# Kernel tuning notes

Hardware: AMD Instinct MI355X
Metric: run time of the kernel (lower is better)

## Reference

```python
import jax, jax.numpy as jnp
import numpy as np

B, S, D = 16, 1024, 512
H = 2048
E = 16
TOP_K = 4


def setup_inputs() -> dict:
    key = jax.random.key(0)
    ks = jax.random.split(key, 8)
    scale = 0.02
    x = jax.random.normal(ks[0], (B, S, D), dtype=jnp.float32)
    router_w = jax.random.normal(ks[1], (D, E), dtype=jnp.float32) * scale
    router_b = jax.random.normal(ks[2], (E,), dtype=jnp.float32) * scale
    w1 = jax.random.normal(ks[3], (E, D, H), dtype=jnp.float32) * scale
    b1 = jax.random.normal(ks[4], (E, H), dtype=jnp.float32) * scale
    w2 = jax.random.normal(ks[5], (E, H, D), dtype=jnp.float32) * scale
    b2 = jax.random.normal(ks[6], (E, D), dtype=jnp.float32) * scale
    return {"x": x, "router_w": router_w, "router_b": router_b,
            "w1": w1, "b1": b1, "w2": w2, "b2": b2}


def reference(x, router_w, router_b, w1, b1, w2, b2):
    # x: [B, S, D] -> flatten tokens
    x_flat = x.reshape(-1, D)                       # [T, D]
    logits = x_flat @ router_w + router_b           # [T, E]
    top_vals, top_idx = jax.lax.top_k(logits, TOP_K)  # [T, K]
    gates = jax.nn.softmax(top_vals, axis=-1)       # softmax over selected experts only
    # Combined per-expert gate weight per token: sum over k slots routed to e.
    onehot = jax.nn.one_hot(top_idx, E, dtype=x.dtype)  # [T, K, E]
    comb = jnp.einsum('tk,tke->te', gates, onehot)      # [T, E]
    out = jnp.zeros_like(x_flat)
    for e in range(E):  # fixed small expert count
        h = jax.nn.relu(x_flat @ w1[e] + b1[e])     # [T, H]
        y = h @ w2[e] + b2[e]                       # [T, D]
        out = out + comb[:, e:e + 1] * y
    return out.reshape(x.shape)
```

## Files before the change

### kernel.cpp

```cpp
#include <hip/hip_runtime.h>
#include <stdint.h>

#define T_TOK 16384
#define DIM 512
#define HID 2048
#define NE 16
#define TOPK 4
#define BM 128
#define BN 128
#define BK 64
#define PAIR_CAP 67584
#define MAX_TILES 528
#define NB_CNT 64

typedef short s8v __attribute__((ext_vector_type(8)));
typedef float f4v __attribute__((ext_vector_type(4)));
typedef unsigned int u4v __attribute__((ext_vector_type(4)));

__device__ __forceinline__ unsigned short f2bf(float f) {
  unsigned int u = __builtin_bit_cast(unsigned int, f);
  u = (u + 0x7fffu + ((u >> 16) & 1u)) >> 16;
  return (unsigned short)u;
}
__device__ __forceinline__ float bf2f(unsigned short h) {
  return __builtin_bit_cast(float, (unsigned int)h << 16);
}

__device__ __forceinline__ void gload16(const void* g, void* l) {
  __builtin_amdgcn_global_load_lds(
      (const __attribute__((address_space(1))) unsigned int*)(uintptr_t)g,
      (__attribute__((address_space(3))) unsigned int*)(uintptr_t)l,
      16, 0, 0);
}

__global__ __launch_bounds__(256) void k_transpose_cast(const float* __restrict__ src,
                                                        unsigned short* __restrict__ dst,
                                                        int R, int C) {
  __shared__ float tile[32][33];
  size_t zo = (size_t)blockIdx.z * R * C;
  src += zo; dst += zo;
  int c0 = blockIdx.x * 32, r0 = blockIdx.y * 32;
  int tx = threadIdx.x, ty = threadIdx.y;
#pragma unroll
  for (int i = 0; i < 4; ++i)
    tile[ty + 8 * i][tx] = src[(size_t)(r0 + ty + 8 * i) * C + c0 + tx];
  __syncthreads();
#pragma unroll
  for (int i = 0; i < 4; ++i)
    dst[(size_t)(c0 + ty + 8 * i) * R + r0 + tx] = f2bf(tile[tx][ty + 8 * i]);
}

__global__ __launch_bounds__(256) void k_router(const float* __restrict__ x,
                                                const float* __restrict__ rw,
                                                const float* __restrict__ rb,
                                                int* __restrict__ topki,
                                                float* __restrict__ topkg,
                                                unsigned short* __restrict__ xb) {
  int wv = threadIdx.x >> 6, lane = threadIdx.x & 63;
  int t = blockIdx.x * 4 + wv;
  const float* xr = x + (size_t)t * DIM;
  unsigned short* xbr = xb + (size_t)t * DIM;
  double acc[NE];
#pragma unroll
  for (int e = 0; e < NE; ++e) acc[e] = 0.0;
  for (int it = 0; it < DIM / 64; ++it) {
    float xv = xr[it * 64 + lane];
    xbr[it * 64 + lane] = f2bf(xv);
    const float* r = rw + (size_t)(it * 64 + lane) * NE;
#pragma unroll
    for (int e = 0; e < NE; ++e) acc[e] += (double)xv * (double)r[e];
  }
#pragma unroll
  for (int off = 32; off >= 1; off >>= 1) {
#pragma unroll
    for (int e = 0; e < NE; ++e) acc[e] += __shfl_xor(acc[e], off, 64);
  }
  if (lane == 0) {
    float v[NE];
#pragma unroll
    for (int e = 0; e < NE; ++e) v[e] = (float)acc[e] + rb[e];
    int idx[TOPK]; float val[TOPK];
#pragma unroll
    for (int k = 0; k < TOPK; ++k) {
      float best = -1e30f; int bi = 0;
#pragma unroll
      for (int e = 0; e < NE; ++e)
        if (v[e] > best) { best = v[e]; bi = e; }
      idx[k] = bi; val[k] = best; v[bi] = -1e30f;
    }
    float m = val[0], s = 0.f, g[TOPK];
#pragma unroll
    for (int k = 0; k < TOPK; ++k) { g[k] = __expf(val[k] - m); s += g[k]; }
    float inv = 1.f / s;
#pragma unroll
    for (int k = 0; k < TOPK; ++k) {
      topki[t * TOPK + k] = idx[k];
      topkg[t * TOPK + k] = g[k] * inv;
    }
  }
}

__global__ __launch_bounds__(256) void k_count(const int* __restrict__ topki,
                                               int* __restrict__ meta) {
  __shared__ int lcnt[NE];
  int tid = threadIdx.x;
  if (tid < NE) lcnt[tid] = 0;
  __syncthreads();
  int base = blockIdx.x * 1024 + tid * 4;
#pragma unroll
  for (int j = 0; j < 4; ++j) atomicAdd(&lcnt[topki[base + j]], 1);
  __syncthreads();
  if (tid < NE) meta[1056 + blockIdx.x * NE + tid] = lcnt[tid];
}

__global__ __launch_bounds__(256) void k_plan(int* __restrict__ meta,
                                              int* __restrict__ ptok,
                                              float* __restrict__ pgate) {
  __shared__ int cnt_s[NE], po_s[NE + 1];
  int tid = threadIdx.x;
  if (tid < NE) {
    int s = 0;
    for (int b = 0; b < NB_CNT; ++b) s += meta[1056 + b * NE + tid];
    cnt_s[tid] = s;
  }
  __syncthreads();
  if (tid == 0) {
    int off = 0;
    for (int e = 0; e < NE; ++e) {
      po_s[e] = off;
      meta[1 + e] = off;
      off += ((cnt_s[e] + BM - 1) / BM) * BM;
    }
    po_s[NE] = off;
    meta[1 + NE] = off;
    meta[0] = off / BM;
  }
  __syncthreads();
  if (tid < NE) {
    int run = po_s[tid];
    for (int b = 0; b < NB_CNT; ++b) {
      meta[32 + b * NE + tid] = run;
      run += meta[1056 + b * NE + tid];
    }
  }
  for (int e = 0; e < NE; ++e) {
    int start = po_s[e] + cnt_s[e], end = po_s[e + 1];
    for (int i = start + tid; i < end; i += 256) { ptok[i] = 0; pgate[i] = 0.f; }
  }
}

__global__ __launch_bounds__(256) void k_scatter(const int* __restrict__ topki,
                                                 const float* __restrict__ topkg,
                                                 const int* __restrict__ meta,
                                                 int* __restrict__ ptok,
                                                 float* __restrict__ pgate,
                                                 int* __restrict__ sinv) {
  __shared__ int lcnt[NE];
  int tid = threadIdx.x;
  if (tid < NE) lcnt[tid] = 0;
  __syncthreads();
  int base = blockIdx.x * 1024 + tid * 4;
#pragma unroll
  for (int j = 0; j < 4; ++j) {
    int i = base + j;
    int e = topki[i];
    int r = atomicAdd(&lcnt[e], 1);
    int slot = meta[32 + blockIdx.x * NE + e] + r;
    ptok[slot] = i >> 2;
    pgate[slot] = topkg[i];
    sinv[i] = slot;
  }
}

__global__ __launch_bounds__(256) void k_pipe(const unsigned short* __restrict__ xb,
                                              const unsigned short* __restrict__ w1t,
                                              const float* __restrict__ b1,
                                              const unsigned short* __restrict__ w2t,
                                              const float* __restrict__ b2,
                                              const int* __restrict__ ptok,
                                              const float* __restrict__ pgate,
                                              const int* __restrict__ meta,
                                              unsigned short* __restrict__ hdst,
                                              const unsigned short* __restrict__ hsrc,
                                              unsigned short* __restrict__ yslot,
                                              float* __restrict__ out,
                                              int c1, int c2, int C) {
  __shared__ __align__(16) unsigned short Al[BM * BK];
  __shared__ __align__(16) unsigned short Bl[BN * BK];
  int tid = threadIdx.x;
  int lane = tid & 63, w = tid >> 6;
  int wm = w >> 1, wn = w & 1;
  int w4 = w * 4096;
  int sub = lane >> 3;
  int lg = (lane & 7) ^ sub;
  int lrow = lane & 15, quad = lane >> 4;
  int r7 = lrow & 7;

  if (blockIdx.x < 16) {
    if (c1 < 0) return;
    int tile = c1 * C + blockIdx.y;
    if (tile >= meta[0]) return;
    int row0 = tile * BM;
    int e = 0;
#pragma unroll
    for (int i = 1; i < NE; ++i)
      if (row0 >= meta[1 + i]) e = i;
    int nblock = blockIdx.x * BN;
    const unsigned short* asrc[4];
    const unsigned short* bsrc[4];
#pragma unroll
    for (int t = 0; t < 4; ++t) {
      int r = w * 32 + t * 8 + sub;
      asrc[t] = xb + (size_t)ptok[row0 + r] * DIM + lg * 8;
      bsrc[t] = w1t + ((size_t)e * HID + nblock + r) * DIM + lg * 8;
    }
    f4v acc[4][4] = {};
    for (int k0 = 0; k0 < DIM; k0 += BK) {
#pragma unroll
      for (int t = 0; t < 4; ++t) gload16(asrc[t] + k0, (char*)Al + w4 + t * 1024);
#pragma unroll
      for (int t = 0; t < 4; ++t) gload16(bsrc[t] + k0, (char*)Bl + w4 + t * 1024);
      __syncthreads();
#pragma unroll
      for (int ks = 0; ks < 2; ++ks) {
        int pg = ((ks * 4 + quad) ^ r7) * 8;
        s8v af[4], bfr[4];
#pragma unroll
        for (int mt = 0; mt < 4; ++mt)
          af[mt] = __builtin_bit_cast(s8v, *(const u4v*)&Al[(wm * 64 + mt * 16 + lrow) * BK + pg]);
#pragma unroll
        for (int nt = 0; nt < 4; ++nt)
          bfr[nt] = __builtin_bit_cast(s8v, *(const u4v*)&Bl[(wn * 64 + nt * 16 + lrow) * BK + pg]);
#pragma unroll
        for (int mt = 0; mt < 4; ++mt) {
#pragma unroll
          for (int nt = 0; nt < 4; ++nt)
            acc[mt][nt] = __builtin_amdgcn_mfma_f32_16x16x32_bf16(af[mt], bfr[nt], acc[mt][nt], 0, 0, 0);
        }
      }
      __syncthreads();
    }
    size_t hrow0 = (size_t)blockIdx.y * BM;
#pragma unroll
    for (int nt = 0; nt < 4; ++nt) {
      int gcol = nblock + wn * 64 + nt * 16 + lrow;
      float bias = b1[e * HID + gcol];
#pragma unroll
      for (int mt = 0; mt < 4; ++mt) {
#pragma unroll
        for (int j = 0; j < 4; ++j) {
          int grow = wm * 64 + mt * 16 + quad * 4 + j;
          float v = acc[mt][nt][j] + bias;
          hdst[(hrow0 + grow) * HID + gcol] = f2bf(v > 0.f ? v : 0.f);
        }
      }
    }
  } else {
    if (c2 < 0) return;
    int tile = c2 * C + blockIdx.y;
    if (tile >= meta[0]) return;
    int row0 = tile * BM;
    int e = 0;
#pragma unroll
    for (int i = 1; i < NE; ++i)
      if (row0 >= meta[1 + i]) e = i;
    int nblock = (blockIdx.x - 16) * BN;
    const unsigned short* asrc[4];
    const unsigned short* bsrc[4];
#pragma unroll
    for (int t = 0; t < 4; ++t) {
      int r = w * 32 + t * 8 + sub;
      asrc[t] = hsrc + ((size_t)blockIdx.y * BM + r) * HID + lg * 8;
      bsrc[t] = w2t + ((size_t)e * DIM + nblock + r) * HID + lg * 8;
    }
    f4v acc[4][4] = {};
    for (int k0 = 0; k0 < HID; k0 += BK) {
#pragma unroll
      for (int t = 0; t < 4; ++t) gload16(asrc[t] + k0, (char*)Al + w4 + t * 1024);
#pragma unroll
      for (int t = 0; t < 4; ++t) gload16(bsrc[t] + k0, (char*)Bl + w4 + t * 1024);
      __syncthreads();
#pragma unroll
      for (int ks = 0; ks < 2; ++ks) {
        int pg = ((ks * 4 + quad) ^ r7) * 8;
        s8v af[4], bfr[4];
#pragma unroll
        for (int mt = 0; mt < 4; ++mt)
          af[mt] = __builtin_bit_cast(s8v, *(const u4v*)&Al[(wm * 64 + mt * 16 + lrow) * BK + pg]);
#pragma unroll
        for (int nt = 0; nt < 4; ++nt)
          bfr[nt] = __builtin_bit_cast(s8v, *(const u4v*)&Bl[(wn * 64 + nt * 16 + lrow) * BK + pg]);
#pragma unroll
        for (int mt = 0; mt < 4; ++mt) {
#pragma unroll
          for (int nt = 0; nt < 4; ++nt)
            acc[mt][nt] = __builtin_amdgcn_mfma_f32_16x16x32_bf16(af[mt], bfr[nt], acc[mt][nt], 0, 0, 0);
        }
      }
      __syncthreads();
    }
    float bias[4];
#pragma unroll
    for (int nt = 0; nt < 4; ++nt)
      bias[nt] = b2[e * DIM + nblock + wn * 64 + nt * 16 + lrow];
    if (yslot) {
#pragma unroll
      for (int mt = 0; mt < 4; ++mt) {
#pragma unroll
        for (int j = 0; j < 4; ++j) {
          int p = row0 + wm * 64 + mt * 16 + quad * 4 + j;
          float g = pgate[p];
          unsigned short* yr = yslot + (size_t)p * DIM + nblock + wn * 64 + lrow;
#pragma unroll
          for (int nt = 0; nt < 4; ++nt)
            yr[nt * 16] = f2bf(g * (acc[mt][nt][j] + bias[nt]));
        }
      }
    } else {
#pragma unroll
      for (int mt = 0; mt < 4; ++mt) {
#pragma unroll
        for (int j = 0; j < 4; ++j) {
          int p = row0 + wm * 64 + mt * 16 + quad * 4 + j;
          float g = pgate[p];
          if (g != 0.f) {
            int tok = ptok[p];
            float* orow = out + (size_t)tok * DIM + nblock + wn * 64 + lrow;
#pragma unroll
            for (int nt = 0; nt < 4; ++nt)
              atomicAdd(orow + nt * 16, g * (acc[mt][nt][j] + bias[nt]));
          }
        }
      }
    }
  }
}

__global__ __launch_bounds__(256) void k_gather(const unsigned short* __restrict__ yslot,
                                                const int* __restrict__ sinv,
                                                float* __restrict__ out) {
  int id = blockIdx.x * 256 + threadIdx.x;
  int t = id >> 7, d4 = (id & 127) << 2;
  int4 s = *(const int4*)(sinv + t * 4);
  int sl[4] = {s.x, s.y, s.z, s.w};
  float sum0 = 0.f, sum1 = 0.f, sum2 = 0.f, sum3 = 0.f;
#pragma unroll
  for (int k = 0; k < 4; ++k) {
    ushort4 v = *(const ushort4*)(yslot + (size_t)sl[k] * DIM + d4);
    sum0 += bf2f(v.x); sum1 += bf2f(v.y); sum2 += bf2f(v.z); sum3 += bf2f(v.w);
  }
  float4 r; r.x = sum0; r.y = sum1; r.z = sum2; r.w = sum3;
  *(float4*)(out + (size_t)t * DIM + d4) = r;
}

extern "C" void kernel_launch(void* const* d_in, const int* in_sizes, int n_in,
                              void* d_out, int out_size, void* d_ws, size_t ws_size,
                              hipStream_t stream) {
  const float* x  = (const float*)d_in[0];
  const float* rw = (const float*)d_in[1];
  const float* rb = (const float*)d_in[2];
  const float* w1 = (const float*)d_in[3];
  const float* b1 = (const float*)d_in[4];
  const float* w2 = (const float*)d_in[5];
  const float* b2 = (const float*)d_in[6];
  float* out = (float*)d_out;
  char* ws = (char*)d_ws;

  size_t o_xb    = 0;
  size_t o_w1t   = o_xb    + (size_t)T_TOK * DIM * 2;
  size_t o_w2t   = o_w1t   + (size_t)NE * DIM * HID * 2;
  size_t o_topki = o_w2t   + (size_t)NE * DIM * HID * 2;
  size_t o_topkg = o_topki + (size_t)T_TOK * TOPK * 4;
  size_t o_meta  = o_topkg + (size_t)T_TOK * TOPK * 4;
  size_t o_ptok  = o_meta  + 16384;
  size_t o_pgate = o_ptok  + (size_t)PAIR_CAP * 4;
  size_t o_sinv  = o_pgate + (size_t)PAIR_CAP * 4;
  size_t o_yslot = o_sinv  + (size_t)T_TOK * TOPK * 4;
  size_t o_hb    = o_yslot + (size_t)PAIR_CAP * DIM * 2;

  unsigned short* xb   = (unsigned short*)(ws + o_xb);
  unsigned short* w1t  = (unsigned short*)(ws + o_w1t);
  unsigned short* w2t  = (unsigned short*)(ws + o_w2t);
  int*            tki  = (int*)(ws + o_topki);
  float*          tkg  = (float*)(ws + o_topkg);
  int*            meta = (int*)(ws + o_meta);
  int*            ptok = (int*)(ws + o_ptok);
  float*          pgt  = (float*)(ws + o_pgate);
  int*            sinv = (int*)(ws + o_sinv);

  size_t tile_h = (size_t)BM * HID * 2;
  size_t avail = ws_size > o_hb ? ws_size - o_hb : 0;
  long Cd = (long)(avail / (2 * tile_h));
  int use_slot = Cd >= 1;

  k_router<<<T_TOK / 4, 256, 0, stream>>>(x, rw, rb, tki, tkg, xb);
  k_transpose_cast<<<dim3(HID / 32, DIM / 32, NE), dim3(32, 8), 0, stream>>>(w1, w1t, DIM, HID);
  k_transpose_cast<<<dim3(DIM / 32, HID / 32, NE), dim3(32, 8), 0, stream>>>(w2, w2t, HID, DIM);
  k_count<<<NB_CNT, 256, 0, stream>>>(tki, meta);
  k_plan<<<1, 256, 0, stream>>>(meta, ptok, pgt);
  k_scatter<<<NB_CNT, 256, 0, stream>>>(tki, tkg, meta, ptok, pgt, sinv);

  if (use_slot) {
    unsigned short* ysl = (unsigned short*)(ws + o_yslot);
    int C = (int)(Cd > MAX_TILES ? MAX_TILES : Cd);
    int n_chunks = (MAX_TILES + C - 1) / C;
    unsigned short* hb0 = (unsigned short*)(ws + o_hb);
    unsigned short* hb1 = hb0 + (size_t)C * BM * HID;
    for (int i = 0; i <= n_chunks; ++i) {
      unsigned short* dst = (i & 1) ? hb1 : hb0;
      unsigned short* src = (i & 1) ? hb0 : hb1;
      int c1 = (i < n_chunks) ? i : -1;
      int c2 = i - 1;
      k_pipe<<<dim3(20, C), 256, 0, stream>>>(xb, w1t, b1, w2t, b2, ptok, pgt, meta,
                                              dst, src, ysl, out, c1, c2, C);
    }
    k_gather<<<T_TOK * DIM / 4 / 256, 256, 0, stream>>>(ysl, sinv, out);
  } else {
    long Cf = (long)((ws_size - o_yslot) / tile_h);
    int C = (int)(Cf < 1 ? 1 : (Cf > MAX_TILES ? MAX_TILES : Cf));
    int n_chunks = (MAX_TILES + C - 1) / C;
    unsigned short* hb = (unsigned short*)(ws + o_yslot);
    hipMemsetAsync(d_out, 0, (size_t)T_TOK * DIM * 4, stream);
    for (int i = 0; i < n_chunks; ++i) {
      k_pipe<<<dim3(20, C), 256, 0, stream>>>(xb, w1t, b1, w2t, b2, ptok, pgt, meta,
                                              hb, hb, nullptr, out, i, -1, C);
      k_pipe<<<dim3(20, C), 256, 0, stream>>>(xb, w1t, b1, w2t, b2, ptok, pgt, meta,
                                              hb, hb, nullptr, out, -1, i, C);
    }
  }
}
```

Baseline: 725.6 us.

## Replace chunked FFN launches with a persistent work-queue kernel and ring buffer

The per-chunk k_pipe launches are replaced by one persistent k_moe kernel of 1024 blocks. Each block takes work items from an atomic counter, and the GEMM2 items for a tile trail the GEMM1 items by LAG tiles. GEMM1 writes ReLU activations into a ring of R tile buffers, and per-tile done counters with acquire/release spin-waits enforce the producer/consumer ordering. This removes the launch boundaries and tail idle time between chunks, so the two GEMM phases can overlap. In exchange it adds spin-wait synchronisation, drops the atomicAdd fallback used when workspace is small, and fails if R becomes zero.

```diff
diff --git a/kernel.cpp b/kernel.cpp
--- a/kernel.cpp
+++ b/kernel.cpp
@@ -13,6 +13,10 @@
 #define MAX_TILES 528
 #define NB_CNT 64
 
+#define MQ_CTR 2080
+#define MQ_G1  2112
+#define MQ_G2  2656
+
 typedef short s8v __attribute__((ext_vector_type(8)));
 typedef float f4v __attribute__((ext_vector_type(4)));
 typedef unsigned int u4v __attribute__((ext_vector_type(4)));
@@ -118,6 +122,7 @@
                                               float* __restrict__ pgate) {
   __shared__ int cnt_s[NE], po_s[NE + 1];
   int tid = threadIdx.x;
+  for (int i = tid; i < 1120; i += 256) meta[MQ_CTR + i] = 0;
   if (tid < NE) {
     int s = 0;
     for (int b = 0; b < NB_CNT; ++b) s += meta[1056 + b * NE + tid];
@@ -172,21 +177,20 @@
   }
 }
 
-__global__ __launch_bounds__(256) void k_pipe(const unsigned short* __restrict__ xb,
-                                              const unsigned short* __restrict__ w1t,
-                                              const float* __restrict__ b1,
-                                              const unsigned short* __restrict__ w2t,
-                                              const float* __restrict__ b2,
-                                              const int* __restrict__ ptok,
-                                              const float* __restrict__ pgate,
-                                              const int* __restrict__ meta,
-                                              unsigned short* __restrict__ hdst,
-                                              const unsigned short* __restrict__ hsrc,
-                                              unsigned short* __restrict__ yslot,
-                                              float* __restrict__ out,
-                                              int c1, int c2, int C) {
+__global__ __launch_bounds__(256, 4) void k_moe(const unsigned short* __restrict__ xb,
+                                                const unsigned short* __restrict__ w1t,
+                                                const float* __restrict__ b1,
+                                                const unsigned short* __restrict__ w2t,
+                                                const float* __restrict__ b2,
+                                                const int* __restrict__ ptok,
+                                                const float* __restrict__ pgate,
+                                                int* meta,
+                                                unsigned short* hring,
+                                                unsigned short* __restrict__ yslot,
+                                                int R, int LAG) {
   __shared__ __align__(16) unsigned short Al[BM * BK];
   __shared__ __align__(16) unsigned short Bl[BN * BK];
+  __shared__ int s_item;
   int tid = threadIdx.x;
   int lane = tid & 63, w = tid >> 6;
   int wm = w >> 1, wn = w & 1;
@@ -195,141 +199,154 @@
   int lg = (lane & 7) ^ sub;
   int lrow = lane & 15, quad = lane >> 4;
   int r7 = lrow & 7;
-
-  if (blockIdx.x < 16) {
-    if (c1 < 0) return;
-    int tile = c1 * C + blockIdx.y;
-    if (tile >= meta[0]) return;
-    int row0 = tile * BM;
-    int e = 0;
-#pragma unroll
-    for (int i = 1; i < NE; ++i)
-      if (row0 >= meta[1 + i]) e = i;
-    int nblock = blockIdx.x * BN;
-    const unsigned short* asrc[4];
-    const unsigned short* bsrc[4];
-#pragma unroll
-    for (int t = 0; t < 4; ++t) {
-      int r = w * 32 + t * 8 + sub;
-      asrc[t] = xb + (size_t)ptok[row0 + r] * DIM + lg * 8;
-      bsrc[t] = w1t + ((size_t)e * HID + nblock + r) * DIM + lg * 8;
-    }
-    f4v acc[4][4] = {};
-    for (int k0 = 0; k0 < DIM; k0 += BK) {
-#pragma unroll
-      for (int t = 0; t < 4; ++t) gload16(asrc[t] + k0, (char*)Al + w4 + t * 1024);
-#pragma unroll
-      for (int t = 0; t < 4; ++t) gload16(bsrc[t] + k0, (char*)Bl + w4 + t * 1024);
+  int tiles = meta[0];
+  int seqlen = (tiles + LAG) * 20;
+  int* g1done = meta + MQ_G1;
+  int* g2done = meta + MQ_G2;
+
+  for (;;) {
+    __syncthreads();
+    if (tid == 0) s_item = atomicAdd(&meta[MQ_CTR], 1);
+    __syncthreads();
+    int p = s_item;
+    if (p >= seqlen) return;
+    int tt = p / 20, r = p % 20;
+    if (r < 16) {
+      if (tt >= tiles) continue;
+      int tile = tt;
+      int row0 = tile * BM;
+      int e = 0;
+#pragma unroll
+      for (int i = 1; i < NE; ++i)
+        if (row0 >= meta[1 + i]) e = i;
+      int nblock = r * BN;
+      const unsigned short* asrc[4];
+      const unsigned short* bsrc[4];
+#pragma unroll
+      for (int t = 0; t < 4; ++t) {
+        int rr = w * 32 + t * 8 + sub;
+        asrc[t] = xb + (size_t)ptok[row0 + rr] * DIM + lg * 8;
+        bsrc[t] = w1t + ((size_t)e * HID + nblock + rr) * DIM + lg * 8;
+      }
+      f4v acc[4][4] = {};
+      for (int k0 = 0; k0 < DIM; k0 += BK) {
+#pragma unroll
+        for (int t = 0; t < 4; ++t) gload16(asrc[t] + k0, (char*)Al + w4 + t * 1024);
+#pragma unroll
+        for (int t = 0; t < 4; ++t) gload16(bsrc[t] + k0, (char*)Bl + w4 + t * 1024);
+        __syncthreads();
+#pragma unroll
+        for (int ks = 0; ks < 2; ++ks) {
+          int pg = ((ks * 4 + quad) ^ r7) * 8;
+          s8v af[4], bfr[4];
+#pragma unroll
+          for (int mt = 0; mt < 4; ++mt)
+            af[mt] = __builtin_bit_cast(s8v, *(const u4v*)&Al[(wm * 64 + mt * 16 + lrow) * BK + pg]);
+#pragma unroll
+          for (int nt = 0; nt < 4; ++nt)
+            bfr[nt] = __builtin_bit_cast(s8v, *(const u4v*)&Bl[(wn * 64 + nt * 16 + lrow) * BK + pg]);
+#pragma unroll
+          for (int mt = 0; mt < 4; ++mt) {
+#pragma unroll
+            for (int nt = 0; nt < 4; ++nt)
+              acc[mt][nt] = __builtin_amdgcn_mfma_f32_16x16x32_bf16(af[mt], bfr[nt], acc[mt][nt], 0, 0, 0);
+          }
+        }
+        __syncthreads();
+      }
+      int prev = tile - R;
+      if (prev >= 0) {
+        if (tid == 0) {
+          while (__hip_atomic_load(&g2done[prev], __ATOMIC_ACQUIRE, __HIP_MEMORY_SCOPE_AGENT) < 4)
+            __builtin_amdgcn_s_sleep(2);
+        }
+        __syncthreads();
+      }
+      unsigned short* hdst = hring + (size_t)(tile % R) * BM * HID;
+#pragma unroll
+      for (int nt = 0; nt < 4; ++nt) {
+        int gcol = nblock + wn * 64 + nt * 16 + lrow;
+        float bias = b1[e * HID + gcol];
+#pragma unroll
+        for (int mt = 0; mt < 4; ++mt) {
+#pragma unroll
+          for (int j = 0; j < 4; ++j) {
+            int grow = wm * 64 + mt * 16 + quad * 4 + j;
+            float v = acc[mt][nt][j] + bias;
+            hdst[(size_t)grow * HID + gcol] = f2bf(v > 0.f ? v : 0.f);
+          }
+        }
+      }
       __syncthreads();
-#pragma unroll
-      for (int ks = 0; ks < 2; ++ks) {
-        int pg = ((ks * 4 + quad) ^ r7) * 8;
-        s8v af[4], bfr[4];
-#pragma unroll
-        for (int mt = 0; mt < 4; ++mt)
-          af[mt] = __builtin_bit_cast(s8v, *(const u4v*)&Al[(wm * 64 + mt * 16 + lrow) * BK + pg]);
-#pragma unroll
-        for (int nt = 0; nt < 4; ++nt)
-          bfr[nt] = __builtin_bit_cast(s8v, *(const u4v*)&Bl[(wn * 64 + nt * 16 + lrow) * BK + pg]);
-#pragma unroll
-        for (int mt = 0; mt < 4; ++mt) {
+      if (tid == 0) {
+        __threadfence();
+        __hip_atomic_fetch_add(&g1done[tile], 1, __ATOMIC_RELEASE, __HIP_MEMORY_SCOPE_AGENT);
+      }
+    } else {
+      int tile = tt - LAG;
+      if (tile < 0 || tile >= tiles) continue;
+      int row0 = tile * BM;
+      int e = 0;
+#pragma unroll
+      for (int i = 1; i < NE; ++i)
+        if (row0 >= meta[1 + i]) e = i;
+      int nblock = (r - 16) * BN;
+      if (tid == 0) {
+        while (__hip_atomic_load(&g1done[tile], __ATOMIC_ACQUIRE, __HIP_MEMORY_SCOPE_AGENT) < 16)
+          __builtin_amdgcn_s_sleep(2);
+      }
+      __syncthreads();
+      const unsigned short* hsrc = hring + (size_t)(tile % R) * BM * HID;
+      const unsigned short* asrc[4];
+      const unsigned short* bsrc[4];
+#pragma unroll
+      for (int t = 0; t < 4; ++t) {
+        int rr = w * 32 + t * 8 + sub;
+        asrc[t] = hsrc + (size_t)rr * HID + lg * 8;
+        bsrc[t] = w2t + ((size_t)e * DIM + nblock + rr) * HID + lg * 8;
+      }
+      f4v acc[4][4] = {};
+      for (int k0 = 0; k0 < HID; k0 += BK) {
+#pragma unroll
+        for (int t = 0; t < 4; ++t) gload16(asrc[t] + k0, (char*)Al + w4 + t * 1024);
+#pragma unroll
+        for (int t = 0; t < 4; ++t) gload16(bsrc[t] + k0, (char*)Bl + w4 + t * 1024);
+        __syncthreads();
+#pragma unroll
+        for (int ks = 0; ks < 2; ++ks) {
+          int pg = ((ks * 4 + quad) ^ r7) * 8;
+          s8v af[4], bfr[4];
+#pragma unroll
+          for (int mt = 0; mt < 4; ++mt)
+            af[mt] = __builtin_bit_cast(s8v, *(const u4v*)&Al[(wm * 64 + mt * 16 + lrow) * BK + pg]);
 #pragma unroll
           for (int nt = 0; nt < 4; ++nt)
-            acc[mt][nt] = __builtin_amdgcn_mfma_f32_16x16x32_bf16(af[mt], bfr[nt], acc[mt][nt], 0, 0, 0);
+            bfr[nt] = __builtin_bit_cast(s8v, *(const u4v*)&Bl[(wn * 64 + nt * 16 + lrow) * BK + pg]);
+#pragma unroll
+          for (int mt = 0; mt < 4; ++mt) {
+#pragma unroll
+            for (int nt = 0; nt < 4; ++nt)
+              acc[mt][nt] = __builtin_amdgcn_mfma_f32_16x16x32_bf16(af[mt], bfr[nt], acc[mt][nt], 0, 0, 0);
+          }
         }
-      }
-      __syncthreads();
-    }
-    size_t hrow0 = (size_t)blockIdx.y * BM;
-#pragma unroll
-    for (int nt = 0; nt < 4; ++nt) {
-      int gcol = nblock + wn * 64 + nt * 16 + lrow;
-      float bias = b1[e * HID + gcol];
+        __syncthreads();
+      }
+      if (tid == 0)
+        __hip_atomic_fetch_add(&g2done[tile], 1, __ATOMIC_RELEASE, __HIP_MEMORY_SCOPE_AGENT);
+      float bias[4];
+#pragma unroll
+      for (int nt = 0; nt < 4; ++nt)
+        bias[nt] = b2[e * DIM + nblock + wn * 64 + nt * 16 + lrow];
 #pragma unroll
       for (int mt = 0; mt < 4; ++mt) {
 #pragma unroll
         for (int j = 0; j < 4; ++j) {
-          int grow = wm * 64 + mt * 16 + quad * 4 + j;
-          float v = acc[mt][nt][j] + bias;
-          hdst[(hrow0 + grow) * HID + gcol] = f2bf(v > 0.f ? v : 0.f);
-        }
-      }
-    }
-  } else {
-    if (c2 < 0) return;
-    int tile = c2 * C + blockIdx.y;
-    if (tile >= meta[0]) return;
-    int row0 = tile * BM;
-    int e = 0;
-#pragma unroll
-    for (int i = 1; i < NE; ++i)
-      if (row0 >= meta[1 + i]) e = i;
-    int nblock = (blockIdx.x - 16) * BN;
-    const unsigned short* asrc[4];
-    const unsigned short* bsrc[4];
-#pragma unroll
-    for (int t = 0; t < 4; ++t) {
-      int r = w * 32 + t * 8 + sub;
-      asrc[t] = hsrc + ((size_t)blockIdx.y * BM + r) * HID + lg * 8;
-      bsrc[t] = w2t + ((size_t)e * DIM + nblock + r) * HID + lg * 8;
-    }
-    f4v acc[4][4] = {};
-    for (int k0 = 0; k0 < HID; k0 += BK) {
-#pragma unroll
-      for (int t = 0; t < 4; ++t) gload16(asrc[t] + k0, (char*)Al + w4 + t * 1024);
-#pragma unroll
-      for (int t = 0; t < 4; ++t) gload16(bsrc[t] + k0, (char*)Bl + w4 + t * 1024);
-      __syncthreads();
-#pragma unroll
-      for (int ks = 0; ks < 2; ++ks) {
-        int pg = ((ks * 4 + quad) ^ r7) * 8;
-        s8v af[4], bfr[4];
-#pragma unroll
-        for (int mt = 0; mt < 4; ++mt)
-          af[mt] = __builtin_bit_cast(s8v, *(const u4v*)&Al[(wm * 64 + mt * 16 + lrow) * BK + pg]);
-#pragma unroll
-        for (int nt = 0; nt < 4; ++nt)
-          bfr[nt] = __builtin_bit_cast(s8v, *(const u4v*)&Bl[(wn * 64 + nt * 16 + lrow) * BK + pg]);
-#pragma unroll
-        for (int mt = 0; mt < 4; ++mt) {
-#pragma unroll
-          for (int nt = 0; nt < 4; ++nt)
-            acc[mt][nt] = __builtin_amdgcn_mfma_f32_16x16x32_bf16(af[mt], bfr[nt], acc[mt][nt], 0, 0, 0);
-        }
-      }
-      __syncthreads();
-    }
-    float bias[4];
-#pragma unroll
-    for (int nt = 0; nt < 4; ++nt)
-      bias[nt] = b2[e * DIM + nblock + wn * 64 + nt * 16 + lrow];
-    if (yslot) {
-#pragma unroll
-      for (int mt = 0; mt < 4; ++mt) {
-#pragma unroll
-        for (int j = 0; j < 4; ++j) {
-          int p = row0 + wm * 64 + mt * 16 + quad * 4 + j;
-          float g = pgate[p];
-          unsigned short* yr = yslot + (size_t)p * DIM + nblock + wn * 64 + lrow;
+          int pp = row0 + wm * 64 + mt * 16 + quad * 4 + j;
+          float g = pgate[pp];
+          unsigned short* yr = yslot + (size_t)pp * DIM + nblock + wn * 64 + lrow;
 #pragma unroll
           for (int nt = 0; nt < 4; ++nt)
             yr[nt * 16] = f2bf(g * (acc[mt][nt][j] + bias[nt]));
-        }
-      }
-    } else {
-#pragma unroll
-      for (int mt = 0; mt < 4; ++mt) {
-#pragma unroll
-        for (int j = 0; j < 4; ++j) {
-          int p = row0 + wm * 64 + mt * 16 + quad * 4 + j;
-          float g = pgate[p];
-          if (g != 0.f) {
-            int tok = ptok[p];
-            float* orow = out + (size_t)tok * DIM + nblock + wn * 64 + lrow;
-#pragma unroll
-            for (int nt = 0; nt < 4; ++nt)
-              atomicAdd(orow + nt * 16, g * (acc[mt][nt][j] + bias[nt]));
-          }
         }
       }
     }
@@ -387,11 +404,15 @@
   int*            ptok = (int*)(ws + o_ptok);
   float*          pgt  = (float*)(ws + o_pgate);
   int*            sinv = (int*)(ws + o_sinv);
+  unsigned short* ysl  = (unsigned short*)(ws + o_yslot);
+  unsigned short* hring = (unsigned short*)(ws + o_hb);
 
   size_t tile_h = (size_t)BM * HID * 2;
   size_t avail = ws_size > o_hb ? ws_size - o_hb : 0;
-  long Cd = (long)(avail / (2 * tile_h));
-  int use_slot = Cd >= 1;
+  long Rl = (long)(avail / tile_h);
+  int R = (int)(Rl > 544 ? 544 : Rl);
+  int LAG = R / 4 < 32 ? R / 4 : 32;
+  int G = 1024;
 
   k_router<<<T_TOK / 4, 256, 0, stream>>>(x, rw, rb, tki, tkg, xb);
   k_transpose_cast<<<dim3(HID / 32, DIM / 32, NE), dim3(32, 8), 0, stream>>>(w1, w1t, DIM, HID);
@@ -399,33 +420,6 @@
   k_count<<<NB_CNT, 256, 0, stream>>>(tki, meta);
   k_plan<<<1, 256, 0, stream>>>(meta, ptok, pgt);
   k_scatter<<<NB_CNT, 256, 0, stream>>>(tki, tkg, meta, ptok, pgt, sinv);
-
-  if (use_slot) {
-    unsigned short* ysl = (unsigned short*)(ws + o_yslot);
-    int C = (int)(Cd > MAX_TILES ? MAX_TILES : Cd);
-    int n_chunks = (MAX_TILES + C - 1) / C;
-    unsigned short* hb0 = (unsigned short*)(ws + o_hb);
-    unsigned short* hb1 = hb0 + (size_t)C * BM * HID;
-    for (int i = 0; i <= n_chunks; ++i) {
-      unsigned short* dst = (i & 1) ? hb1 : hb0;
-      unsigned short* src = (i & 1) ? hb0 : hb1;
-      int c1 = (i < n_chunks) ? i : -1;
-      int c2 = i - 1;
-      k_pipe<<<dim3(20, C), 256, 0, stream>>>(xb, w1t, b1, w2t, b2, ptok, pgt, meta,
-                                              dst, src, ysl, out, c1, c2, C);
-    }
-    k_gather<<<T_TOK * DIM / 4 / 256, 256, 0, stream>>>(ysl, sinv, out);
-  } else {
-    long Cf = (long)((ws_size - o_yslot) / tile_h);
-    int C = (int)(Cf < 1 ? 1 : (Cf > MAX_TILES ? MAX_TILES : Cf));
-    int n_chunks = (MAX_TILES + C - 1) / C;
-    unsigned short* hb = (unsigned short*)(ws + o_yslot);
-    hipMemsetAsync(d_out, 0, (size_t)T_TOK * DIM * 4, stream);
-    for (int i = 0; i < n_chunks; ++i) {
-      k_pipe<<<dim3(20, C), 256, 0, stream>>>(xb, w1t, b1, w2t, b2, ptok, pgt, meta,
-                                              hb, hb, nullptr, out, i, -1, C);
-      k_pipe<<<dim3(20, C), 256, 0, stream>>>(xb, w1t, b1, w2t, b2, ptok, pgt, meta,
-                                              hb, hb, nullptr, out, -1, i, C);
-    }
-  }
-}
+  k_moe<<<G, 256, 0, stream>>>(xb, w1t, b1, w2t, b2, ptok, pgt, meta, hring, ysl, R, LAG);
+  k_gather<<<T_TOK * DIM / 4 / 256, 256, 0, stream>>>(ysl, sinv, out);
+}
```

Measured after the change: 2.148 ms. 196% more time.
